# Optimization experiments

Hardware: AMD Instinct MI355X
Metric: run time of the kernel (lower is better)

The kernel has to match this reference:

```python
import jax, jax.numpy as jnp
import numpy as np

D_MODEL, JOINT_DIM, VOCAB = 512, 640, 1024
B, T, U = 4, 256, 64


def setup_inputs() -> dict:
    key = jax.random.key(0)
    ks = jax.random.split(key, 8)
    s_in = 1.0 / np.sqrt(D_MODEL)
    s_j = 1.0 / np.sqrt(JOINT_DIM)
    return {
        "enc": jax.random.normal(ks[0], (B, T, D_MODEL), jnp.float32),
        "pred": jax.random.normal(ks[1], (B, U, D_MODEL), jnp.float32),
        "enc_w": jax.random.uniform(ks[2], (JOINT_DIM, D_MODEL), jnp.float32, -s_in, s_in),
        "enc_b": jax.random.uniform(ks[3], (JOINT_DIM,), jnp.float32, -s_in, s_in),
        "pred_w": jax.random.uniform(ks[4], (JOINT_DIM, D_MODEL), jnp.float32, -s_in, s_in),
        "pred_b": jax.random.uniform(ks[5], (JOINT_DIM,), jnp.float32, -s_in, s_in),
        "out_w": jax.random.uniform(ks[6], (VOCAB, JOINT_DIM), jnp.float32, -s_j, s_j),
        "out_b": jax.random.uniform(ks[7], (VOCAB,), jnp.float32, -s_j, s_j),
    }


def reference(enc, pred, enc_w, enc_b, pred_w, pred_b, out_w, out_b):
    # project encoder (B,T,J) and predictor (B,U,J)
    e = jnp.einsum("btd,jd->btj", enc, enc_w) + enc_b
    p = jnp.einsum("bud,jd->buj", pred, pred_w) + pred_b
    # broadcast add over the (T,U) grid, tanh, then vocab projection
    z = jnp.tanh(e[:, :, None, :] + p[:, None, :, :])  # (B,T,U,J)
    logits = jnp.einsum("btuj,vj->btuv", z, out_w) + out_b  # (B,T,U,V)
    return logits
```

## Files before the change

kernel.cpp:

```cpp
#include <hip/hip_runtime.h>
#include <cstdint>
#include <cstddef>


typedef __attribute__((ext_vector_type(8))) __bf16 bf16x8;
typedef __attribute__((ext_vector_type(4))) float f32x4;

__device__ __forceinline__ int swz64(int row, int kElem) {
  return (row << 6) + (kElem ^ ((row & 7) << 3));
}

__device__ __forceinline__ float fast_tanh(float x) {
  float e = __builtin_amdgcn_exp2f(x * 2.88539008177793f);
  return 1.0f - 2.0f * __builtin_amdgcn_rcpf(e + 1.0f);
}

__device__ __forceinline__ void gload_lds16(const void* g, void* l) {
  __builtin_amdgcn_global_load_lds(
      (const __attribute__((address_space(1))) void*)g,
      (__attribute__((address_space(3))) void*)l, 16, 0, 0);
}

__device__ void proj_tile(const float* __restrict__ A, const float* __restrict__ W,
                          const float* __restrict__ bias, __bf16* __restrict__ C,
                          int mt, int nt, __bf16* As, __bf16* Bs)
{
  const int tid  = threadIdx.x;
  const int r = tid & 127, half = tid >> 7;
  const int lane = tid & 63, wv = tid >> 6;
  const int wm = wv >> 1, wn = wv & 1;

  const float* arow = A + (size_t)(mt * 128 + r) * 512 + half * 32;
  const float* wrow = W + (size_t)(nt * 128 + r) * 512 + half * 32;

  f32x4 acc[4][4] = {};

  for (int k0 = 0; k0 < 512; k0 += 64) {
#pragma unroll
    for (int s = 0; s < 4; ++s) {
      f32x4 a0 = *(const f32x4*)(arow + k0 + s * 8);
      f32x4 a1 = *(const f32x4*)(arow + k0 + s * 8 + 4);
      f32x4 w0 = *(const f32x4*)(wrow + k0 + s * 8);
      f32x4 w1 = *(const f32x4*)(wrow + k0 + s * 8 + 4);
      bf16x8 za, zw;
#pragma unroll
      for (int j = 0; j < 4; ++j) {
        za[j] = (__bf16)a0[j]; za[4 + j] = (__bf16)a1[j];
        zw[j] = (__bf16)w0[j]; zw[4 + j] = (__bf16)w1[j];
      }
      const int kk = half * 32 + s * 8;
      *(bf16x8*)&As[swz64(r, kk)] = za;
      *(bf16x8*)&Bs[swz64(r, kk)] = zw;
    }
    __syncthreads();
#pragma unroll
    for (int kk = 0; kk < 2; ++kk) {
      bf16x8 af[4], bfr[4];
#pragma unroll
      for (int i = 0; i < 4; ++i) {
        af[i]  = *(const bf16x8*)&As[swz64(wm * 64 + i * 16 + (lane & 15), kk * 32 + (lane >> 4) * 8)];
        bfr[i] = *(const bf16x8*)&Bs[swz64(wn * 64 + i * 16 + (lane & 15), kk * 32 + (lane >> 4) * 8)];
      }
#pragma unroll
      for (int mi = 0; mi < 4; ++mi)
#pragma unroll
        for (int ni = 0; ni < 4; ++ni)
          acc[mi][ni] = __builtin_amdgcn_mfma_f32_16x16x32_bf16(af[mi], bfr[ni], acc[mi][ni], 0, 0, 0);
    }
    __syncthreads();
  }

  const int rowbase = mt * 128 + wm * 64;
  const int colbase = nt * 128 + wn * 64;
#pragma unroll
  for (int ni = 0; ni < 4; ++ni) {
    const int col = colbase + ni * 16 + (lane & 15);
    const float bb = bias[col];
#pragma unroll
    for (int mi = 0; mi < 4; ++mi) {
      const int row = rowbase + mi * 16 + (lane >> 4) * 4;
#pragma unroll
      for (int rg = 0; rg < 4; ++rg)
        C[(size_t)(row + rg) * 640 + col] = (__bf16)(acc[mi][ni][rg] + bb);
    }
  }
}

__global__ __launch_bounds__(256) void prep_kernel(
    const float* __restrict__ enc,  const float* __restrict__ enc_w,  const float* __restrict__ enc_b,
    const float* __restrict__ pred, const float* __restrict__ pred_w, const float* __restrict__ pred_b,
    const float* __restrict__ out_w,
    __bf16* __restrict__ E, __bf16* __restrict__ P, __bf16* __restrict__ Wb, int zpath)
{
  __shared__ __align__(16) __bf16 As[128 * 64];
  __shared__ __align__(16) __bf16 Bs[128 * 64];
  const int bid = blockIdx.x;
  if (bid < 40) {
    proj_tile(enc, enc_w, enc_b, E, bid / 5, bid % 5, As, Bs);
  } else if (bid < 50) {
    proj_tile(pred, pred_w, pred_b, P, (bid - 40) / 5, (bid - 40) % 5, As, Bs);
  } else {
    const int gid = (bid - 50) * 256 + threadIdx.x;
    const int v  = gid / 80;
    const int j8 = gid % 80;
    f32x4 w0 = *(const f32x4*)(out_w + (size_t)v * 640 + j8 * 8);
    f32x4 w1 = *(const f32x4*)(out_w + (size_t)v * 640 + j8 * 8 + 4);
    bf16x8 z;
#pragma unroll
    for (int j = 0; j < 4; ++j) { z[j] = (__bf16)w0[j]; z[4 + j] = (__bf16)w1[j]; }
    if (zpath) {
      const int nt = v >> 8, vv = v & 255;
      const int half = vv >> 7, rr = vv & 127;
      const int kt = j8 >> 3, kk = (j8 & 7) * 8;
      *(bf16x8*)(Wb + (((size_t)(nt * 10 + kt) * 2 + half) << 13) + swz64(rr, kk)) = z;
    } else {
      const int nb = v >> 7, rr = v & 127;
      const int kb = j8 >> 3, kk = (j8 & 7) * 8;
      *(bf16x8*)(Wb + ((size_t)(nb * 10 + kb) << 13) + swz64(rr, kk)) = z;
    }
  }
}

__global__ __launch_bounds__(256) void zprod_kernel(
    const __bf16* __restrict__ E, const __bf16* __restrict__ P,
    __bf16* __restrict__ Z)
{
  const int bid = blockIdx.x;
  const int mt = bid / 10, kt = bid % 10;
  __bf16* zdst = Z + ((size_t)bid << 14);

#pragma unroll
  for (int c = 0; c < 8; ++c) {
    const int o = c * 2048 + threadIdx.x * 8;
    const int half = o >> 13, oo = o & 8191;
    const int rr = oo >> 6;
    const int r = half * 128 + rr;
    const int k = kt * 64 + ((oo & 63) ^ ((rr & 7) << 3));
    const int grow = mt * 256 + r;
    const __bf16* ep = E + (size_t)(grow >> 6) * 640 + k;
    const __bf16* pp = P + (size_t)(((grow >> 14) << 6) | (grow & 63)) * 640 + k;
    bf16x8 e8 = *(const bf16x8*)ep;
    bf16x8 p8 = *(const bf16x8*)pp;
    bf16x8 z;
#pragma unroll
    for (int j = 0; j < 8; ++j)
      z[j] = (__bf16)fast_tanh((float)e8[j] + (float)p8[j]);
    *(bf16x8*)&zdst[o] = z;
  }
}

__global__ __launch_bounds__(512, 2) void joiner_8p(
    const __bf16* __restrict__ Z, const __bf16* __restrict__ Wb,
    const float* __restrict__ outb, float* __restrict__ out)
{
  __shared__ __align__(16) __bf16 As[2][2][8192];
  __shared__ __align__(16) __bf16 Bs[2][2][8192];
  const int wg = blockIdx.x;
  const int bid = (wg & 7) * 128 + (wg >> 3);
  const int mt = bid >> 2, nt = bid & 3;
  const int tid = threadIdx.x;
  const int lane = tid & 63, wv = tid >> 6;
  const int wm = wv >> 2, wn = wv & 3;

  const int rb  = wm * 16 + (lane & 15);
  const int cb  = wn * 16 + (lane & 15);
  const int kb8 = (lane >> 4) * 8;

  const __bf16* zsrc = Z  + ((size_t)(mt * 20) << 13);
  const __bf16* wsrc = Wb + ((size_t)(nt * 20) << 13);

  f32x4 acc[8][4] = {};

  auto stA = [&](int kt, int half) {
    __bf16* dst = &As[kt & 1][half][wv * 512];
    const __bf16* src = zsrc + (((size_t)kt * 2 + half) << 13) + wv * 512 + lane * 8;
    gload_lds16(src, dst);
    gload_lds16(src + 4096, dst + 4096);
  };
  auto stB = [&](int kt, int half) {
    __bf16* dst = &Bs[kt & 1][half][wv * 512];
    const __bf16* src = wsrc + (((size_t)kt * 2 + half) << 13) + wv * 512 + lane * 8;
    gload_lds16(src, dst);
    gload_lds16(src + 4096, dst + 4096);
  };

  stA(0, 0); stB(0, 0); stB(0, 1); stA(0, 1);
  stA(1, 0); stB(1, 0); stB(1, 1);
  asm volatile("s_waitcnt vmcnt(6)" ::: "memory");
  __builtin_amdgcn_s_barrier();

#pragma unroll
  for (int k = 0; k < 10; ++k) {
    const int d = k & 1;
    const __bf16* A0 = &As[d][0][0];
    const __bf16* A1 = &As[d][1][0];
    const __bf16* B0 = &Bs[d][0][0];
    const __bf16* B1 = &Bs[d][1][0];
    bf16x8 afl[4][2], afh[4][2], bl[2][2], bh[2][2];

#pragma unroll
    for (int f = 0; f < 4; ++f)
#pragma unroll
      for (int kk = 0; kk < 2; ++kk)
        afl[f][kk] = *(const bf16x8*)&A0[swz64(f * 32 + rb, kk * 32 + kb8)];
#pragma unroll
    for (int g = 0; g < 2; ++g)
#pragma unroll
      for (int kk = 0; kk < 2; ++kk)
        bl[g][kk] = *(const bf16x8*)&B0[swz64(g * 64 + cb, kk * 32 + kb8)];
    if (k < 9) stA(k + 1, 1);
    if (k == 9) asm volatile("s_waitcnt vmcnt(0)" ::: "memory");
    else        asm volatile("s_waitcnt vmcnt(6)" ::: "memory");
    __builtin_amdgcn_s_barrier();
    asm volatile("s_waitcnt lgkmcnt(0)" ::: "memory");
    __builtin_amdgcn_sched_barrier(0);
    __builtin_amdgcn_s_setprio(1);
#pragma unroll
    for (int kk = 0; kk < 2; ++kk)
#pragma unroll
      for (int f = 0; f < 4; ++f)
#pragma unroll
        for (int g = 0; g < 2; ++g)
          acc[f][g] = __builtin_amdgcn_mfma_f32_16x16x32_bf16(afl[f][kk], bl[g][kk], acc[f][g], 0, 0, 0);
    __builtin_amdgcn_s_setprio(0);
    __builtin_amdgcn_s_barrier();

#pragma unroll
    for (int g = 0; g < 2; ++g)
#pragma unroll
      for (int kk = 0; kk < 2; ++kk)
        bh[g][kk] = *(const bf16x8*)&B1[swz64(g * 64 + cb, kk * 32 + kb8)];
    if (k < 8) stA(k + 2, 0);
    __builtin_amdgcn_s_barrier();
    asm volatile("s_waitcnt lgkmcnt(0)" ::: "memory");
    __builtin_amdgcn_sched_barrier(0);
    __builtin_amdgcn_s_setprio(1);
#pragma unroll
    for (int kk = 0; kk < 2; ++kk)
#pragma unroll
      for (int f = 0; f < 4; ++f)
#pragma unroll
        for (int g = 0; g < 2; ++g)
          acc[f][2 + g] = __builtin_amdgcn_mfma_f32_16x16x32_bf16(afl[f][kk], bh[g][kk], acc[f][2 + g], 0, 0, 0);
    __builtin_amdgcn_s_setprio(0);
    __builtin_amdgcn_s_barrier();

#pragma unroll
    for (int f = 0; f < 4; ++f)
#pragma unroll
      for (int kk = 0; kk < 2; ++kk)
        afh[f][kk] = *(const bf16x8*)&A1[swz64(f * 32 + rb, kk * 32 + kb8)];
    if (k < 8) stB(k + 2, 0);
    __builtin_amdgcn_s_barrier();
    asm volatile("s_waitcnt lgkmcnt(0)" ::: "memory");
    __builtin_amdgcn_sched_barrier(0);
    __builtin_amdgcn_s_setprio(1);
#pragma unroll
    for (int kk = 0; kk < 2; ++kk)
#pragma unroll
      for (int f = 0; f < 4; ++f)
#pragma unroll
        for (int g = 0; g < 2; ++g)
          acc[4 + f][2 + g] = __builtin_amdgcn_mfma_f32_16x16x32_bf16(afh[f][kk], bh[g][kk], acc[4 + f][2 + g], 0, 0, 0);
    __builtin_amdgcn_s_setprio(0);
    __builtin_amdgcn_s_barrier();

    if (k < 8) stB(k + 2, 1);
    __builtin_amdgcn_s_setprio(1);
#pragma unroll
    for (int kk = 0; kk < 2; ++kk)
#pragma unroll
      for (int f = 0; f < 4; ++f)
#pragma unroll
        for (int g = 0; g < 2; ++g)
          acc[4 + f][g] = __builtin_amdgcn_mfma_f32_16x16x32_bf16(afh[f][kk], bl[g][kk], acc[4 + f][g], 0, 0, 0);
    __builtin_amdgcn_s_setprio(0);
  }

  const int rowbase = (mt << 8) + wm * 16 + (lane >> 4) * 4;
  const int colbase = (nt << 8) + wn * 16 + (lane & 15);
#pragma unroll
  for (int g = 0; g < 4; ++g) {
    const int col = colbase + g * 64;
    const float bb = outb[col];
#pragma unroll
    for (int f = 0; f < 8; ++f) {
      const int row = rowbase + f * 32;
#pragma unroll
      for (int rg = 0; rg < 4; ++rg)
        out[(size_t)(row + rg) * 1024 + col] = acc[f][g][rg] + bb;
    }
  }
}

__global__ __launch_bounds__(512, 4) void joiner_fused(
    const __bf16* __restrict__ E, const __bf16* __restrict__ P,
    const __bf16* __restrict__ Wb, const float* __restrict__ outb,
    float* __restrict__ out)
{
  __shared__ __align__(16) __bf16 As[8192];
  __shared__ __align__(16) __bf16 Bs[2][16384];
  const int tid = threadIdx.x;
  const int nt = blockIdx.x & 3;
  const int mt = blockIdx.x >> 2;
  const int row0 = mt << 7;
  const int b  = row0 >> 14;
  const int t0 = (row0 >> 6) & 255;
  const int ar = tid & 127, h = tid >> 7;
  const int lane = tid & 63, wv = tid >> 6;
  const int wm = wv >> 2, wn = wv & 3;

  const __bf16* ep = E + (size_t)((b << 8) + t0 + (ar >> 6)) * 640 + h * 16;
  const __bf16* pp = P + (size_t)((b << 6) + (ar & 63)) * 640 + h * 16;

  f32x4 acc[4][4] = {};
  bf16x8 eA[2], pA[2];

  auto stageB2 = [&](int kt, __bf16* dst) {
#pragma unroll
    for (int c = 0; c < 4; ++c) {
      const int blk = nt * 2 + (c >> 1);
      const int inoff = (c & 1) * 4096 + wv * 512;
      gload_lds16(Wb + ((size_t)(blk * 10 + kt) << 13) + inoff + lane * 8,
                  dst + (c >> 1) * 8192 + inoff);
    }
  };
  auto loadEP = [&](int k0) {
#pragma unroll
    for (int c = 0; c < 2; ++c) {
      eA[c] = *(const bf16x8*)(ep + k0 + c * 8);
      pA[c] = *(const bf16x8*)(pp + k0 + c * 8);
    }
  };
  auto writeA = [&]() {
#pragma unroll
    for (int c = 0; c < 2; ++c) {
      bf16x8 z;
#pragma unroll
      for (int j = 0; j < 8; ++j)
        z[j] = (__bf16)fast_tanh((float)eA[c][j] + (float)pA[c][j]);
      *(bf16x8*)&As[swz64(ar, h * 16 + c * 8)] = z;
    }
  };
  auto compute = [&](const __bf16* Bsc) {
#pragma unroll
    for (int kk = 0; kk < 2; ++kk) {
      bf16x8 af[4], bfr[4];
#pragma unroll
      for (int i = 0; i < 4; ++i) {
        af[i]  = *(const bf16x8*)&As[swz64(wm * 64 + i * 16 + (lane & 15), kk * 32 + (lane >> 4) * 8)];
        bfr[i] = *(const bf16x8*)&Bsc[swz64(wn * 64 + i * 16 + (lane & 15), kk * 32 + (lane >> 4) * 8)];
      }
      asm volatile("s_waitcnt lgkmcnt(0)" ::: "memory");
      __builtin_amdgcn_sched_barrier(0);
      __builtin_amdgcn_s_setprio(1);
#pragma unroll
      for (int mi = 0; mi < 4; ++mi)
#pragma unroll
        for (int ni = 0; ni < 4; ++ni)
          acc[mi][ni] = __builtin_amdgcn_mfma_f32_16x16x32_bf16(af[mi], bfr[ni], acc[mi][ni], 0, 0, 0);
      __builtin_amdgcn_s_setprio(0);
    }
  };

  stageB2(0, Bs[0]);
  loadEP(0);
  writeA();
  asm volatile("s_waitcnt vmcnt(0) lgkmcnt(0)" ::: "memory");
  __builtin_amdgcn_s_barrier();

  for (int kt = 0; kt < 9; ++kt) {
    const int cur = kt & 1;
    stageB2(kt + 1, Bs[cur ^ 1]);
    loadEP((kt + 1) << 6);
    compute(Bs[cur]);
    __builtin_amdgcn_s_barrier();
    __builtin_amdgcn_sched_barrier(0);
    writeA();
    asm volatile("s_waitcnt lgkmcnt(0)" ::: "memory");
    __builtin_amdgcn_s_barrier();
  }
  compute(Bs[1]);

  const int rowbase = row0 + wm * 64;
  const int colbase = (nt << 8) + wn * 64;
#pragma unroll
  for (int ni = 0; ni < 4; ++ni) {
    const int col = colbase + ni * 16 + (lane & 15);
    const float bb = outb[col];
#pragma unroll
    for (int mi = 0; mi < 4; ++mi) {
      const int row = rowbase + mi * 16 + (lane >> 4) * 4;
#pragma unroll
      for (int rg = 0; rg < 4; ++rg)
        out[(size_t)(row + rg) * 1024 + col] = acc[mi][ni][rg] + bb;
    }
  }
}

extern "C" void kernel_launch(void* const* d_in, const int* in_sizes, int n_in,
                              void* d_out, int out_size, void* d_ws, size_t ws_size,
                              hipStream_t stream) {
  const float* enc    = (const float*)d_in[0];
  const float* pred   = (const float*)d_in[1];
  const float* enc_w  = (const float*)d_in[2];
  const float* enc_b  = (const float*)d_in[3];
  const float* pred_w = (const float*)d_in[4];
  const float* pred_b = (const float*)d_in[5];
  const float* out_w  = (const float*)d_in[6];
  const float* out_b  = (const float*)d_in[7];
  float* out = (float*)d_out;

  char* ws = (char*)d_ws;
  __bf16* E  = (__bf16*)(ws);
  __bf16* P  = (__bf16*)(ws + 1310720);
  __bf16* Wb = (__bf16*)(ws + 1638400);
  __bf16* Z  = (__bf16*)(ws + 2949120);

  const int zpath = (ws_size >= (size_t)86835200) ? 1 : 0;

  prep_kernel<<<dim3(370), dim3(256), 0, stream>>>(
      enc, enc_w, enc_b, pred, pred_w, pred_b, out_w, E, P, Wb, zpath);

  if (zpath) {
    zprod_kernel<<<dim3(2560), dim3(256), 0, stream>>>(E, P, Z);
    joiner_8p<<<dim3(1024), dim3(512), 0, stream>>>(Z, Wb, out_b, out);
  } else {
    joiner_fused<<<dim3(2048), dim3(512), 0, stream>>>(E, P, Wb, out_b, out);
  }
}
```

Baseline: 154.5 us.

## Make joiner GEMM persistent over four M tiles with cross-tile prefetch

The zpath joiner kernel now launches 256 workgroups, each processing four consecutive 256-row M tiles for one N tile. It prefetches the next tile's first K slices during the last iterations of the current tile, so the pipeline does not drain and refill between tiles. Accumulators are initialised with the bias, which removes the add in the epilogue. The launch drops from four waves of blocks to one, which cuts launch and prologue overhead but risks load imbalance across CUs, and the per-tile output store still sits between compute phases.

```diff
diff --git a/kernel.cpp b/kernel.cpp
--- a/kernel.cpp
+++ b/kernel.cpp
@@ -19,6 +19,12 @@
   __builtin_amdgcn_global_load_lds(
       (const __attribute__((address_space(1))) void*)g,
       (__attribute__((address_space(3))) void*)l, 16, 0, 0);
+}
+
+__device__ __forceinline__ void wg_barrier() {
+  asm volatile("" ::: "memory");
+  __builtin_amdgcn_s_barrier();
+  asm volatile("" ::: "memory");
 }
 
 __device__ void proj_tile(const float* __restrict__ A, const float* __restrict__ W,
@@ -149,15 +155,15 @@
   }
 }
 
-__global__ __launch_bounds__(512, 2) void joiner_8p(
+__global__ __launch_bounds__(512, 2) void joiner_8pm(
     const __bf16* __restrict__ Z, const __bf16* __restrict__ Wb,
     const float* __restrict__ outb, float* __restrict__ out)
 {
   __shared__ __align__(16) __bf16 As[2][2][8192];
   __shared__ __align__(16) __bf16 Bs[2][2][8192];
   const int wg = blockIdx.x;
-  const int bid = (wg & 7) * 128 + (wg >> 3);
-  const int mt = bid >> 2, nt = bid & 3;
+  const int bid = (wg & 7) * 32 + (wg >> 3);
+  const int nt = bid & 3, mtg = bid >> 2;
   const int tid = threadIdx.x;
   const int lane = tid & 63, wv = tid >> 6;
   const int wm = wv >> 2, wn = wv & 3;
@@ -166,14 +172,25 @@
   const int cb  = wn * 16 + (lane & 15);
   const int kb8 = (lane >> 4) * 8;
 
-  const __bf16* zsrc = Z  + ((size_t)(mt * 20) << 13);
+  const size_t ZSTRIDE = (size_t)20 << 13;
+  const __bf16* zc = Z + (size_t)(mtg * 4) * ZSTRIDE;
   const __bf16* wsrc = Wb + ((size_t)(nt * 20) << 13);
 
-  f32x4 acc[8][4] = {};
-
-  auto stA = [&](int kt, int half) {
+  const int colbase = (nt << 8) + wn * 16 + (lane & 15);
+  float bv[4];
+#pragma unroll
+  for (int g = 0; g < 4; ++g) bv[g] = outb[colbase + g * 64];
+
+  f32x4 acc[8][4];
+#pragma unroll
+  for (int f = 0; f < 8; ++f)
+#pragma unroll
+    for (int g = 0; g < 4; ++g)
+      acc[f][g] = (f32x4){bv[g], bv[g], bv[g], bv[g]};
+
+  auto stA = [&](const __bf16* zp, int kt, int half) {
     __bf16* dst = &As[kt & 1][half][wv * 512];
-    const __bf16* src = zsrc + (((size_t)kt * 2 + half) << 13) + wv * 512 + lane * 8;
+    const __bf16* src = zp + (((size_t)kt * 2 + half) << 13) + wv * 512 + lane * 8;
     gload_lds16(src, dst);
     gload_lds16(src + 4096, dst + 4096);
   };
@@ -184,111 +201,126 @@
     gload_lds16(src + 4096, dst + 4096);
   };
 
-  stA(0, 0); stB(0, 0); stB(0, 1); stA(0, 1);
-  stA(1, 0); stB(1, 0); stB(1, 1);
+  stA(zc, 0, 0); stB(0, 0); stB(0, 1); stA(zc, 0, 1);
+  stA(zc, 1, 0); stB(1, 0); stB(1, 1);
   asm volatile("s_waitcnt vmcnt(6)" ::: "memory");
-  __builtin_amdgcn_s_barrier();
-
-#pragma unroll
-  for (int k = 0; k < 10; ++k) {
-    const int d = k & 1;
-    const __bf16* A0 = &As[d][0][0];
-    const __bf16* A1 = &As[d][1][0];
-    const __bf16* B0 = &Bs[d][0][0];
-    const __bf16* B1 = &Bs[d][1][0];
-    bf16x8 afl[4][2], afh[4][2], bl[2][2], bh[2][2];
-
-#pragma unroll
-    for (int f = 0; f < 4; ++f)
+  wg_barrier();
+
+  for (int i = 0; i < 4; ++i, zc += ZSTRIDE) {
+    const __bf16* zn = zc + ZSTRIDE;
+    const int last = (i == 3);
+
+#pragma unroll
+    for (int k = 0; k < 10; ++k) {
+      const int d = k & 1;
+      const __bf16* A0 = &As[d][0][0];
+      const __bf16* A1 = &As[d][1][0];
+      const __bf16* B0 = &Bs[d][0][0];
+      const __bf16* B1 = &Bs[d][1][0];
+      bf16x8 afl[4][2], afh[4][2], bl[2][2], bh[2][2];
+
+#pragma unroll
+      for (int f = 0; f < 4; ++f)
+#pragma unroll
+        for (int kk = 0; kk < 2; ++kk)
+          afl[f][kk] = *(const bf16x8*)&A0[swz64(f * 32 + rb, kk * 32 + kb8)];
+#pragma unroll
+      for (int g = 0; g < 2; ++g)
+#pragma unroll
+        for (int kk = 0; kk < 2; ++kk)
+          bl[g][kk] = *(const bf16x8*)&B0[swz64(g * 64 + cb, kk * 32 + kb8)];
+      if (k < 9)      stA(zc, k + 1, 1);
+      else if (!last) stA(zn, 0, 1);
+      if (k == 9 && last) asm volatile("s_waitcnt vmcnt(0)" ::: "memory");
+      else                asm volatile("s_waitcnt vmcnt(6)" ::: "memory");
+      wg_barrier();
+      asm volatile("s_waitcnt lgkmcnt(0)" ::: "memory");
+      __builtin_amdgcn_sched_barrier(0);
+      __builtin_amdgcn_s_setprio(1);
 #pragma unroll
       for (int kk = 0; kk < 2; ++kk)
-        afl[f][kk] = *(const bf16x8*)&A0[swz64(f * 32 + rb, kk * 32 + kb8)];
-#pragma unroll
-    for (int g = 0; g < 2; ++g)
+#pragma unroll
+        for (int f = 0; f < 4; ++f)
+#pragma unroll
+          for (int g = 0; g < 2; ++g)
+            acc[f][g] = __builtin_amdgcn_mfma_f32_16x16x32_bf16(afl[f][kk], bl[g][kk], acc[f][g], 0, 0, 0);
+      __builtin_amdgcn_s_setprio(0);
+      wg_barrier();
+
+#pragma unroll
+      for (int g = 0; g < 2; ++g)
+#pragma unroll
+        for (int kk = 0; kk < 2; ++kk)
+          bh[g][kk] = *(const bf16x8*)&B1[swz64(g * 64 + cb, kk * 32 + kb8)];
+      if (k < 8)      stA(zc, k + 2, 0);
+      else if (!last) stA(zn, k - 8, 0);
+      wg_barrier();
+      asm volatile("s_waitcnt lgkmcnt(0)" ::: "memory");
+      __builtin_amdgcn_sched_barrier(0);
+      __builtin_amdgcn_s_setprio(1);
 #pragma unroll
       for (int kk = 0; kk < 2; ++kk)
-        bl[g][kk] = *(const bf16x8*)&B0[swz64(g * 64 + cb, kk * 32 + kb8)];
-    if (k < 9) stA(k + 1, 1);
-    if (k == 9) asm volatile("s_waitcnt vmcnt(0)" ::: "memory");
-    else        asm volatile("s_waitcnt vmcnt(6)" ::: "memory");
-    __builtin_amdgcn_s_barrier();
-    asm volatile("s_waitcnt lgkmcnt(0)" ::: "memory");
-    __builtin_amdgcn_sched_barrier(0);
-    __builtin_amdgcn_s_setprio(1);
-#pragma unroll
-    for (int kk = 0; kk < 2; ++kk)
+#pragma unroll
+        for (int f = 0; f < 4; ++f)
+#pragma unroll
+          for (int g = 0; g < 2; ++g)
+            acc[f][2 + g] = __builtin_amdgcn_mfma_f32_16x16x32_bf16(afl[f][kk], bh[g][kk], acc[f][2 + g], 0, 0, 0);
+      __builtin_amdgcn_s_setprio(0);
+      wg_barrier();
+
 #pragma unroll
       for (int f = 0; f < 4; ++f)
 #pragma unroll
-        for (int g = 0; g < 2; ++g)
-          acc[f][g] = __builtin_amdgcn_mfma_f32_16x16x32_bf16(afl[f][kk], bl[g][kk], acc[f][g], 0, 0, 0);
-    __builtin_amdgcn_s_setprio(0);
-    __builtin_amdgcn_s_barrier();
-
-#pragma unroll
-    for (int g = 0; g < 2; ++g)
+        for (int kk = 0; kk < 2; ++kk)
+          afh[f][kk] = *(const bf16x8*)&A1[swz64(f * 32 + rb, kk * 32 + kb8)];
+      if (k < 8)      stB(k + 2, 0);
+      else if (!last) stB(k - 8, 0);
+      wg_barrier();
+      asm volatile("s_waitcnt lgkmcnt(0)" ::: "memory");
+      __builtin_amdgcn_sched_barrier(0);
+      __builtin_amdgcn_s_setprio(1);
 #pragma unroll
       for (int kk = 0; kk < 2; ++kk)
-        bh[g][kk] = *(const bf16x8*)&B1[swz64(g * 64 + cb, kk * 32 + kb8)];
-    if (k < 8) stA(k + 2, 0);
-    __builtin_amdgcn_s_barrier();
-    asm volatile("s_waitcnt lgkmcnt(0)" ::: "memory");
-    __builtin_amdgcn_sched_barrier(0);
-    __builtin_amdgcn_s_setprio(1);
-#pragma unroll
-    for (int kk = 0; kk < 2; ++kk)
-#pragma unroll
-      for (int f = 0; f < 4; ++f)
-#pragma unroll
-        for (int g = 0; g < 2; ++g)
-          acc[f][2 + g] = __builtin_amdgcn_mfma_f32_16x16x32_bf16(afl[f][kk], bh[g][kk], acc[f][2 + g], 0, 0, 0);
-    __builtin_amdgcn_s_setprio(0);
-    __builtin_amdgcn_s_barrier();
-
-#pragma unroll
-    for (int f = 0; f < 4; ++f)
+#pragma unroll
+        for (int f = 0; f < 4; ++f)
+#pragma unroll
+          for (int g = 0; g < 2; ++g)
+            acc[4 + f][2 + g] = __builtin_amdgcn_mfma_f32_16x16x32_bf16(afh[f][kk], bh[g][kk], acc[4 + f][2 + g], 0, 0, 0);
+      __builtin_amdgcn_s_setprio(0);
+      wg_barrier();
+
+      if (k < 8)      stB(k + 2, 1);
+      else if (!last) stB(k - 8, 1);
+      __builtin_amdgcn_s_setprio(1);
 #pragma unroll
       for (int kk = 0; kk < 2; ++kk)
-        afh[f][kk] = *(const bf16x8*)&A1[swz64(f * 32 + rb, kk * 32 + kb8)];
-    if (k < 8) stB(k + 2, 0);
-    __builtin_amdgcn_s_barrier();
-    asm volatile("s_waitcnt lgkmcnt(0)" ::: "memory");
-    __builtin_amdgcn_sched_barrier(0);
-    __builtin_amdgcn_s_setprio(1);
-#pragma unroll
-    for (int kk = 0; kk < 2; ++kk)
-#pragma unroll
-      for (int f = 0; f < 4; ++f)
-#pragma unroll
-        for (int g = 0; g < 2; ++g)
-          acc[4 + f][2 + g] = __builtin_amdgcn_mfma_f32_16x16x32_bf16(afh[f][kk], bh[g][kk], acc[4 + f][2 + g], 0, 0, 0);
-    __builtin_amdgcn_s_setprio(0);
-    __builtin_amdgcn_s_barrier();
-
-    if (k < 8) stB(k + 2, 1);
-    __builtin_amdgcn_s_setprio(1);
-#pragma unroll
-    for (int kk = 0; kk < 2; ++kk)
-#pragma unroll
-      for (int f = 0; f < 4; ++f)
-#pragma unroll
-        for (int g = 0; g < 2; ++g)
-          acc[4 + f][g] = __builtin_amdgcn_mfma_f32_16x16x32_bf16(afh[f][kk], bl[g][kk], acc[4 + f][g], 0, 0, 0);
-    __builtin_amdgcn_s_setprio(0);
-  }
-
-  const int rowbase = (mt << 8) + wm * 16 + (lane >> 4) * 4;
-  const int colbase = (nt << 8) + wn * 16 + (lane & 15);
-#pragma unroll
-  for (int g = 0; g < 4; ++g) {
-    const int col = colbase + g * 64;
-    const float bb = outb[col];
-#pragma unroll
-    for (int f = 0; f < 8; ++f) {
-      const int row = rowbase + f * 32;
-#pragma unroll
-      for (int rg = 0; rg < 4; ++rg)
-        out[(size_t)(row + rg) * 1024 + col] = acc[f][g][rg] + bb;
+#pragma unroll
+        for (int f = 0; f < 4; ++f)
+#pragma unroll
+          for (int g = 0; g < 2; ++g)
+            acc[4 + f][g] = __builtin_amdgcn_mfma_f32_16x16x32_bf16(afh[f][kk], bl[g][kk], acc[4 + f][g], 0, 0, 0);
+      __builtin_amdgcn_s_setprio(0);
+      wg_barrier();
+    }
+
+    const int rowbase = ((mtg * 4 + i) << 8) + wm * 16 + (lane >> 4) * 4;
+#pragma unroll
+    for (int g = 0; g < 4; ++g) {
+      const int col = colbase + g * 64;
+#pragma unroll
+      for (int f = 0; f < 8; ++f) {
+        const int row = rowbase + f * 32;
+#pragma unroll
+        for (int rg = 0; rg < 4; ++rg)
+          out[(size_t)(row + rg) * 1024 + col] = acc[f][g][rg];
+      }
+    }
+    if (i < 3) {
+#pragma unroll
+      for (int f = 0; f < 8; ++f)
+#pragma unroll
+        for (int g = 0; g < 4; ++g)
+          acc[f][g] = (f32x4){bv[g], bv[g], bv[g], bv[g]};
     }
   }
 }
@@ -367,18 +399,18 @@
   loadEP(0);
   writeA();
   asm volatile("s_waitcnt vmcnt(0) lgkmcnt(0)" ::: "memory");
-  __builtin_amdgcn_s_barrier();
+  wg_barrier();
 
   for (int kt = 0; kt < 9; ++kt) {
     const int cur = kt & 1;
     stageB2(kt + 1, Bs[cur ^ 1]);
     loadEP((kt + 1) << 6);
     compute(Bs[cur]);
-    __builtin_amdgcn_s_barrier();
+    wg_barrier();
     __builtin_amdgcn_sched_barrier(0);
     writeA();
     asm volatile("s_waitcnt lgkmcnt(0)" ::: "memory");
-    __builtin_amdgcn_s_barrier();
+    wg_barrier();
   }
   compute(Bs[1]);
 
@@ -424,7 +456,7 @@
 
   if (zpath) {
     zprod_kernel<<<dim3(2560), dim3(256), 0, stream>>>(E, P, Z);
-    joiner_8p<<<dim3(1024), dim3(512), 0, stream>>>(Z, Wb, out_b, out);
+    joiner_8pm<<<dim3(256), dim3(512), 0, stream>>>(Z, Wb, out_b, out);
   } else {
     joiner_fused<<<dim3(2048), dim3(512), 0, stream>>>(E, P, Wb, out_b, out);
   }
```

After: 250.8 us. +62.3%, slower.

## Software-pipeline LDS fragment reads across phases in the joiner GEMM loop

Applied to the files above, without the earlier changes.

Reorders the 8-phase joiner main loop so the next tile's A-low fragments are read during the last MFMA phase of the current iteration. Both B halves are issued together, and partial lgkmcnt waits let MFMAs start before every LDS read has landed. Barriers are wrapped with compiler memory fences so the reads are not moved across them. The aim is to hide LDS read latency behind MFMA work, at the cost of more live registers and an extra barrier at the end of each iteration.

```diff
diff --git a/kernel.cpp b/kernel.cpp
--- a/kernel.cpp
+++ b/kernel.cpp
@@ -19,6 +19,12 @@
   __builtin_amdgcn_global_load_lds(
       (const __attribute__((address_space(1))) void*)g,
       (__attribute__((address_space(3))) void*)l, 16, 0, 0);
+}
+
+__device__ __forceinline__ void wg_barrier() {
+  asm volatile("" ::: "memory");
+  __builtin_amdgcn_s_barrier();
+  asm volatile("" ::: "memory");
 }
 
 __device__ void proj_tile(const float* __restrict__ A, const float* __restrict__ W,
@@ -149,7 +155,7 @@
   }
 }
 
-__global__ __launch_bounds__(512, 2) void joiner_8p(
+__global__ __launch_bounds__(512, 2) void joiner_8pr(
     const __bf16* __restrict__ Z, const __bf16* __restrict__ Wb,
     const float* __restrict__ outb, float* __restrict__ out)
 {
@@ -170,6 +176,7 @@
   const __bf16* wsrc = Wb + ((size_t)(nt * 20) << 13);
 
   f32x4 acc[8][4] = {};
+  bf16x8 afl[4][2], afh[4][2], bl[2][2], bh[2][2];
 
   auto stA = [&](int kt, int half) {
     __bf16* dst = &As[kt & 1][half][wv * 512];
@@ -183,36 +190,51 @@
     gload_lds16(src, dst);
     gload_lds16(src + 4096, dst + 4096);
   };
+  auto rdAfl = [&](const __bf16* A0) {
+#pragma unroll
+    for (int f = 0; f < 4; ++f)
+#pragma unroll
+      for (int kk = 0; kk < 2; ++kk)
+        afl[f][kk] = *(const bf16x8*)&A0[swz64(f * 32 + rb, kk * 32 + kb8)];
+  };
+  auto rdAfh = [&](const __bf16* A1) {
+#pragma unroll
+    for (int f = 0; f < 4; ++f)
+#pragma unroll
+      for (int kk = 0; kk < 2; ++kk)
+        afh[f][kk] = *(const bf16x8*)&A1[swz64(f * 32 + rb, kk * 32 + kb8)];
+  };
 
   stA(0, 0); stB(0, 0); stB(0, 1); stA(0, 1);
   stA(1, 0); stB(1, 0); stB(1, 1);
   asm volatile("s_waitcnt vmcnt(6)" ::: "memory");
-  __builtin_amdgcn_s_barrier();
-
-#pragma unroll
-  for (int k = 0; k < 10; ++k) {
-    const int d = k & 1;
-    const __bf16* A0 = &As[d][0][0];
+  wg_barrier();
+  rdAfl(&As[0][0][0]);
+  __builtin_amdgcn_sched_barrier(0);
+
+#pragma unroll
+  for (int t = 0; t < 10; ++t) {
+    const int d = t & 1;
     const __bf16* A1 = &As[d][1][0];
     const __bf16* B0 = &Bs[d][0][0];
     const __bf16* B1 = &Bs[d][1][0];
-    bf16x8 afl[4][2], afh[4][2], bl[2][2], bh[2][2];
-
-#pragma unroll
-    for (int f = 0; f < 4; ++f)
-#pragma unroll
-      for (int kk = 0; kk < 2; ++kk)
-        afl[f][kk] = *(const bf16x8*)&A0[swz64(f * 32 + rb, kk * 32 + kb8)];
+
+    if (t < 9) stA(t + 1, 1);
+    if (t == 9) asm volatile("s_waitcnt vmcnt(0)" ::: "memory");
+    else        asm volatile("s_waitcnt vmcnt(6)" ::: "memory");
+    wg_barrier();
 #pragma unroll
     for (int g = 0; g < 2; ++g)
 #pragma unroll
       for (int kk = 0; kk < 2; ++kk)
         bl[g][kk] = *(const bf16x8*)&B0[swz64(g * 64 + cb, kk * 32 + kb8)];
-    if (k < 9) stA(k + 1, 1);
-    if (k == 9) asm volatile("s_waitcnt vmcnt(0)" ::: "memory");
-    else        asm volatile("s_waitcnt vmcnt(6)" ::: "memory");
-    __builtin_amdgcn_s_barrier();
-    asm volatile("s_waitcnt lgkmcnt(0)" ::: "memory");
+    __builtin_amdgcn_sched_barrier(0);
+#pragma unroll
+    for (int g = 0; g < 2; ++g)
+#pragma unroll
+      for (int kk = 0; kk < 2; ++kk)
+        bh[g][kk] = *(const bf16x8*)&B1[swz64(g * 64 + cb, kk * 32 + kb8)];
+    asm volatile("s_waitcnt lgkmcnt(4)" ::: "memory");
     __builtin_amdgcn_sched_barrier(0);
     __builtin_amdgcn_s_setprio(1);
 #pragma unroll
@@ -223,16 +245,13 @@
         for (int g = 0; g < 2; ++g)
           acc[f][g] = __builtin_amdgcn_mfma_f32_16x16x32_bf16(afl[f][kk], bl[g][kk], acc[f][g], 0, 0, 0);
     __builtin_amdgcn_s_setprio(0);
-    __builtin_amdgcn_s_barrier();
-
-#pragma unroll
-    for (int g = 0; g < 2; ++g)
-#pragma unroll
-      for (int kk = 0; kk < 2; ++kk)
-        bh[g][kk] = *(const bf16x8*)&B1[swz64(g * 64 + cb, kk * 32 + kb8)];
-    if (k < 8) stA(k + 2, 0);
-    __builtin_amdgcn_s_barrier();
-    asm volatile("s_waitcnt lgkmcnt(0)" ::: "memory");
+    wg_barrier();
+
+    rdAfh(A1);
+    __builtin_amdgcn_sched_barrier(0);
+    if (t < 8) stA(t + 2, 0);
+    wg_barrier();
+    asm volatile("s_waitcnt lgkmcnt(8)" ::: "memory");
     __builtin_amdgcn_sched_barrier(0);
     __builtin_amdgcn_s_setprio(1);
 #pragma unroll
@@ -243,15 +262,10 @@
         for (int g = 0; g < 2; ++g)
           acc[f][2 + g] = __builtin_amdgcn_mfma_f32_16x16x32_bf16(afl[f][kk], bh[g][kk], acc[f][2 + g], 0, 0, 0);
     __builtin_amdgcn_s_setprio(0);
-    __builtin_amdgcn_s_barrier();
-
-#pragma unroll
-    for (int f = 0; f < 4; ++f)
-#pragma unroll
-      for (int kk = 0; kk < 2; ++kk)
-        afh[f][kk] = *(const bf16x8*)&A1[swz64(f * 32 + rb, kk * 32 + kb8)];
-    if (k < 8) stB(k + 2, 0);
-    __builtin_amdgcn_s_barrier();
+    wg_barrier();
+
+    if (t < 8) stB(t + 2, 0);
+    wg_barrier();
     asm volatile("s_waitcnt lgkmcnt(0)" ::: "memory");
     __builtin_amdgcn_sched_barrier(0);
     __builtin_amdgcn_s_setprio(1);
@@ -263,9 +277,11 @@
         for (int g = 0; g < 2; ++g)
           acc[4 + f][2 + g] = __builtin_amdgcn_mfma_f32_16x16x32_bf16(afh[f][kk], bh[g][kk], acc[4 + f][2 + g], 0, 0, 0);
     __builtin_amdgcn_s_setprio(0);
-    __builtin_amdgcn_s_barrier();
-
-    if (k < 8) stB(k + 2, 1);
+    wg_barrier();
+
+    if (t < 8) stB(t + 2, 1);
+    if (t < 9) rdAfl(&As[(t + 1) & 1][0][0]);
+    __builtin_amdgcn_sched_barrier(0);
     __builtin_amdgcn_s_setprio(1);
 #pragma unroll
     for (int kk = 0; kk < 2; ++kk)
@@ -275,6 +291,7 @@
         for (int g = 0; g < 2; ++g)
           acc[4 + f][g] = __builtin_amdgcn_mfma_f32_16x16x32_bf16(afh[f][kk], bl[g][kk], acc[4 + f][g], 0, 0, 0);
     __builtin_amdgcn_s_setprio(0);
+    wg_barrier();
   }
 
   const int rowbase = (mt << 8) + wm * 16 + (lane >> 4) * 4;
@@ -367,18 +384,18 @@
   loadEP(0);
   writeA();
   asm volatile("s_waitcnt vmcnt(0) lgkmcnt(0)" ::: "memory");
-  __builtin_amdgcn_s_barrier();
+  wg_barrier();
 
   for (int kt = 0; kt < 9; ++kt) {
     const int cur = kt & 1;
     stageB2(kt + 1, Bs[cur ^ 1]);
     loadEP((kt + 1) << 6);
     compute(Bs[cur]);
-    __builtin_amdgcn_s_barrier();
+    wg_barrier();
     __builtin_amdgcn_sched_barrier(0);
     writeA();
     asm volatile("s_waitcnt lgkmcnt(0)" ::: "memory");
-    __builtin_amdgcn_s_barrier();
+    wg_barrier();
   }
   compute(Bs[1]);
 
@@ -424,7 +441,7 @@
 
   if (zpath) {
     zprod_kernel<<<dim3(2560), dim3(256), 0, stream>>>(E, P, Z);
-    joiner_8p<<<dim3(1024), dim3(512), 0, stream>>>(Z, Wb, out_b, out);
+    joiner_8pr<<<dim3(1024), dim3(512), 0, stream>>>(Z, Wb, out_b, out);
   } else {
     joiner_fused<<<dim3(2048), dim3(512), 0, stream>>>(E, P, Wb, out_b, out);
   }
```

Result: no change. 155.8 us (+0.8%).
